# Kernel tuning notes

Hardware: AMD Instinct MI355X
Metric: run time of the kernel (lower is better)

The kernel has to match this reference:

```python
import jax, jax.numpy as jnp
import numpy as np

MAX_OBJECTS = 65536
K = 8            # slots_per_object
D = 256          # d_memory
M = 65536        # number of objects stored this frame (unique indices)


def setup_inputs() -> dict:
    key = jax.random.key(0)
    k1, k2, k3, k4, k5 = jax.random.split(key, 5)
    return {
        "memory": jax.random.normal(k1, (MAX_OBJECTS, K, D), dtype=jnp.float32),
        "capture_poses": jax.random.normal(k2, (MAX_OBJECTS, K, 4, 4), dtype=jnp.float32),
        "slot_filled": jnp.zeros((MAX_OBJECTS, K), dtype=bool),
        "slot_count": jax.random.randint(k3, (MAX_OBJECTS,), 0, 9, dtype=jnp.int32),
        "object_indices": jnp.arange(M, dtype=jnp.int32),
        "features": jax.random.normal(k4, (M, D), dtype=jnp.float32),
        "camera_pose": jax.random.normal(k5, (4, 4), dtype=jnp.float32),
    }


def _pose_deltas(camera_pose, stored_poses):
    # camera_pose: (4,4); stored_poses: (M,K,4,4) -> deltas (M,K)
    R_curr = camera_pose[:3, :3]               # (3,3)
    t_curr = camera_pose[:3, 3]                # (3,)
    R_s = stored_poses[:, :, :3, :3]           # (M,K,3,3)
    t_s = stored_poses[:, :, :3, 3]            # (M,K,3)
    # R_curr @ R_s^T per (m,k): [i,l] = sum_j R_curr[i,j] * R_s[m,k,l,j]
    R_diff = jnp.einsum('ij,mklj->mkil', R_curr, R_s)
    eye = jnp.eye(3, dtype=R_diff.dtype)
    rot_delta = jnp.linalg.norm((R_diff - eye).reshape(*R_diff.shape[:2], 9), axis=-1)
    trans_delta = jnp.linalg.norm(t_curr - t_s, axis=-1)
    return rot_delta + trans_delta             # (M,K)


def reference(memory, capture_poses, slot_filled, slot_count, object_indices, features, camera_pose):
    """Vectorized equivalent of store(): per object, fill next slot if not full,
    else evict the slot with the most similar capture pose. Indices are unique,
    so all M updates are independent and match the sequential torch loop."""
    k = memory.shape[1]
    cnt = slot_count[object_indices]                      # (M,)
    stored = capture_poses[object_indices]                # (M,K,4,4)
    deltas = _pose_deltas(camera_pose, stored)            # (M,K)
    evict_slot = jnp.argmin(deltas, axis=-1).astype(cnt.dtype)
    fill_branch = cnt < k                                 # (M,) bool
    slot = jnp.where(fill_branch, cnt, evict_slot)        # (M,)

    mem_new = memory.at[object_indices, slot].set(features)
    poses_new = capture_poses.at[object_indices, slot].set(camera_pose)
    filled_new = slot_filled.at[object_indices, slot].set(True)
    count_new = slot_count.at[object_indices].add(fill_branch.astype(slot_count.dtype))
    return mem_new, poses_new, filled_new, count_new
```

## Files before the change

### kernel.cpp

```cpp
#include <hip/hip_runtime.h>

#define MAXOBJ 65536
#define KSLOTS 8
#define DFEAT 256

typedef float f32x4 __attribute__((ext_vector_type(4)));


__global__ void init_slots_kernel(int* __restrict__ slots, int n) {
    int i = blockIdx.x * blockDim.x + threadIdx.x;
    if (i < n) slots[i] = -1;
}

__global__ void slot_compute_kernel(const float* __restrict__ capture_poses,
                                    const int* __restrict__ slot_count,
                                    const int* __restrict__ object_indices,
                                    const float* __restrict__ camera_pose,
                                    int* __restrict__ slots,
                                    int* __restrict__ srcs,
                                    int M) {
    int m = blockIdx.x * blockDim.x + threadIdx.x;
    if (m >= M) return;
    int obj = object_indices[m];

    float Rc[3][3], tc[3];
#pragma unroll
    for (int i = 0; i < 3; i++) {
        Rc[i][0] = camera_pose[i * 4 + 0];
        Rc[i][1] = camera_pose[i * 4 + 1];
        Rc[i][2] = camera_pose[i * 4 + 2];
        tc[i]    = camera_pose[i * 4 + 3];
    }

    int cnt = slot_count[obj];
    const float* ps = capture_poses + (size_t)obj * (KSLOTS * 16);

    float best = 3.4e38f;
    int bestk = 0;
#pragma unroll
    for (int k = 0; k < KSLOTS; k++) {
        const float* p = ps + k * 16;
        float rot = 0.f;
#pragma unroll
        for (int i = 0; i < 3; i++) {
#pragma unroll
            for (int l = 0; l < 3; l++) {
                float v = Rc[i][0] * p[l * 4 + 0] + Rc[i][1] * p[l * 4 + 1] + Rc[i][2] * p[l * 4 + 2];
                v -= (i == l) ? 1.f : 0.f;
                rot += v * v;
            }
        }
        float tx = tc[0] - p[3];
        float ty = tc[1] - p[7];
        float tz = tc[2] - p[11];
        float delta = sqrtf(rot) + sqrtf(tx * tx + ty * ty + tz * tz);
        if (delta < best) { best = delta; bestk = k; }
    }

    int fill = (cnt < KSLOTS) ? 1 : 0;
    int slot = fill ? cnt : bestk;
    slots[obj] = slot;
    srcs[obj] = m;
}

__global__ void fused_copy_kernel(const f32x4* __restrict__ memory,
                                  const f32x4* __restrict__ features,
                                  const f32x4* __restrict__ capture_poses,
                                  const f32x4* __restrict__ camera_pose,
                                  const unsigned char* __restrict__ slot_filled,
                                  const int* __restrict__ slot_count,
                                  const int* __restrict__ slots,
                                  const int* __restrict__ srcs,
                                  f32x4* __restrict__ mem_out,
                                  f32x4* __restrict__ poses_out,
                                  float* __restrict__ filled_out,
                                  float* __restrict__ count_out) {
    const int obj = blockIdx.x;
    const int t = threadIdx.x;
    const int slot = slots[obj];
    const int src  = srcs[obj];

    const size_t base = (size_t)obj * (KSLOTS * DFEAT / 4);
    const int d4 = t & 63;

    {
        const int k = t >> 6;
        f32x4 v;
        if (k == slot) {
            v = features[(size_t)src * (DFEAT / 4) + d4];
        } else {
            v = __builtin_nontemporal_load(&memory[base + t]);
        }
        __builtin_nontemporal_store(v, &mem_out[base + t]);
    }
    {
        const int k = 4 + (t >> 6);
        f32x4 v;
        if (k == slot) {
            v = features[(size_t)src * (DFEAT / 4) + d4];
        } else {
            v = __builtin_nontemporal_load(&memory[base + 256 + t]);
        }
        __builtin_nontemporal_store(v, &mem_out[base + 256 + t]);
    }

    if (t < 32) {
        const int k  = t >> 2;
        const int r4 = t & 3;
        const size_t pbase = (size_t)obj * (KSLOTS * 16 / 4);
        f32x4 v = (k == slot) ? camera_pose[r4] : capture_poses[pbase + t];
        poses_out[pbase + t] = v;
    }

    if (t >= 64 && t < 64 + KSLOTS) {
        const int k = t - 64;
        int was = slot_filled[obj * KSLOTS + k] != 0;
        filled_out[obj * KSLOTS + k] = (was || k == slot) ? 1.0f : 0.0f;
    }

    if (t == 96) {
        int cnt = slot_count[obj];
        int fill = (slot >= 0 && cnt < KSLOTS) ? 1 : 0;
        count_out[obj] = (float)(cnt + fill);
    }
}

extern "C" void kernel_launch(void* const* d_in, const int* in_sizes, int n_in,
                              void* d_out, int out_size, void* d_ws, size_t ws_size,
                              hipStream_t stream) {
    const float*         memory        = (const float*)d_in[0];
    const float*         capture_poses = (const float*)d_in[1];
    const unsigned char* slot_filled   = (const unsigned char*)d_in[2];
    const int*           slot_count    = (const int*)d_in[3];
    const int*           object_indices= (const int*)d_in[4];
    const float*         features      = (const float*)d_in[5];
    const float*         camera_pose   = (const float*)d_in[6];
    const int M = in_sizes[4];

    float* out = (float*)d_out;
    float* mem_out    = out;
    float* poses_out  = out + (size_t)MAXOBJ * KSLOTS * DFEAT;
    float* filled_out = poses_out + (size_t)MAXOBJ * KSLOTS * 16;
    float* count_out  = filled_out + (size_t)MAXOBJ * KSLOTS;

    int* slots = (int*)d_ws;
    int* srcs  = slots + MAXOBJ;

    const int B = 256;

    init_slots_kernel<<<(MAXOBJ + B - 1) / B, B, 0, stream>>>(slots, MAXOBJ);

    slot_compute_kernel<<<(M + B - 1) / B, B, 0, stream>>>(
        capture_poses, slot_count, object_indices, camera_pose, slots, srcs, M);

    fused_copy_kernel<<<MAXOBJ, B, 0, stream>>>(
        (const f32x4*)memory, (const f32x4*)features,
        (const f32x4*)capture_poses, (const f32x4*)camera_pose,
        slot_filled, slot_count, slots, srcs,
        (f32x4*)mem_out, (f32x4*)poses_out, filled_out, count_out);
}
```

Measured before the change: 209.9 us.

## Fuse slot selection into copy kernel with warp-shuffle argmin

```diff
diff --git a/kernel.cpp b/kernel.cpp
--- a/kernel.cpp
+++ b/kernel.cpp
@@ -7,121 +7,114 @@
 typedef float f32x4 __attribute__((ext_vector_type(4)));
 
 
-__global__ void init_slots_kernel(int* __restrict__ slots, int n) {
+__global__ void init_srcs_kernel(int* __restrict__ srcs, int n) {
     int i = blockIdx.x * blockDim.x + threadIdx.x;
-    if (i < n) slots[i] = -1;
+    if (i < n) srcs[i] = -1;
 }
 
-__global__ void slot_compute_kernel(const float* __restrict__ capture_poses,
-                                    const int* __restrict__ slot_count,
-                                    const int* __restrict__ object_indices,
-                                    const float* __restrict__ camera_pose,
-                                    int* __restrict__ slots,
-                                    int* __restrict__ srcs,
-                                    int M) {
+__global__ void scatter_srcs_kernel(const int* __restrict__ object_indices,
+                                    int* __restrict__ srcs, int M) {
     int m = blockIdx.x * blockDim.x + threadIdx.x;
-    if (m >= M) return;
-    int obj = object_indices[m];
+    if (m < M) srcs[object_indices[m]] = m;
+}
 
-    float Rc[3][3], tc[3];
+__global__ void fused_kernel(const f32x4* __restrict__ memory,
+                             const f32x4* __restrict__ features,
+                             const f32x4* __restrict__ capture_poses,
+                             const float* __restrict__ camera_pose,
+                             const unsigned char* __restrict__ slot_filled,
+                             const int* __restrict__ slot_count,
+                             const int* __restrict__ srcs,
+                             f32x4* __restrict__ mem_out,
+                             f32x4* __restrict__ poses_out,
+                             float* __restrict__ filled_out,
+                             float* __restrict__ count_out) {
+    const int obj = blockIdx.x;
+    const int t = threadIdx.x;
+    const int src = srcs[obj];
+    const int d4 = t & 63;
+
+    f32x4 feat = {0.f, 0.f, 0.f, 0.f};
+    if (src >= 0) feat = features[(size_t)src * (DFEAT / 4) + d4];
+
+    __shared__ int s_slot;
+
+    if (t < 32) {
+        const int k  = t >> 2;
+        const int r4 = t & 3;
+        const size_t pbase = (size_t)obj * (KSLOTS * 16 / 4);
+        f32x4 pv = capture_poses[pbase + t];
+
+        float Rc00 = camera_pose[0],  Rc01 = camera_pose[1],  Rc02 = camera_pose[2];
+        float Rc10 = camera_pose[4],  Rc11 = camera_pose[5],  Rc12 = camera_pose[6];
+        float Rc20 = camera_pose[8],  Rc21 = camera_pose[9],  Rc22 = camera_pose[10];
+        float tc0 = camera_pose[3], tc1 = camera_pose[7], tc2 = camera_pose[11];
+
+        float rot_part = 0.f, tr_part = 0.f;
+        if (r4 < 3) {
+            float v0 = Rc00 * pv.x + Rc01 * pv.y + Rc02 * pv.z - (r4 == 0 ? 1.f : 0.f);
+            float v1 = Rc10 * pv.x + Rc11 * pv.y + Rc12 * pv.z - (r4 == 1 ? 1.f : 0.f);
+            float v2 = Rc20 * pv.x + Rc21 * pv.y + Rc22 * pv.z - (r4 == 2 ? 1.f : 0.f);
+            rot_part = v0 * v0 + v1 * v1 + v2 * v2;
+            float tcur = (r4 == 0) ? tc0 : (r4 == 1) ? tc1 : tc2;
+            float dt = tcur - pv.w;
+            tr_part = dt * dt;
+        }
+        rot_part += __shfl_xor(rot_part, 1);
+        tr_part  += __shfl_xor(tr_part, 1);
+        rot_part += __shfl_xor(rot_part, 2);
+        tr_part  += __shfl_xor(tr_part, 2);
+        float delta = sqrtf(rot_part) + sqrtf(tr_part);
+
+        int bestk = k;
+        float bestd = delta;
 #pragma unroll
-    for (int i = 0; i < 3; i++) {
-        Rc[i][0] = camera_pose[i * 4 + 0];
-        Rc[i][1] = camera_pose[i * 4 + 1];
-        Rc[i][2] = camera_pose[i * 4 + 2];
-        tc[i]    = camera_pose[i * 4 + 3];
+        for (int mask = 4; mask <= 16; mask <<= 1) {
+            float od = __shfl_xor(bestd, mask);
+            int   ok = __shfl_xor(bestk, mask);
+            if (od < bestd || (od == bestd && ok < bestk)) { bestd = od; bestk = ok; }
+        }
+
+        const int cnt = slot_count[obj];
+        const int fill = (cnt < KSLOTS) ? 1 : 0;
+        const int slot = (src < 0) ? -1 : (fill ? cnt : bestk);
+
+        if (t == 0) {
+            s_slot = slot;
+            count_out[obj] = (float)(cnt + ((src >= 0) ? fill : 0));
+        }
+        if (t < KSLOTS) {
+            int was = slot_filled[obj * KSLOTS + t] != 0;
+            filled_out[obj * KSLOTS + t] = (was || t == slot) ? 1.0f : 0.0f;
+        }
+        f32x4 pov;
+        if (k == slot) {
+            const f32x4* cp4 = (const f32x4*)camera_pose;
+            pov = cp4[r4];
+        } else {
+            pov = pv;
+        }
+        __builtin_nontemporal_store(pov, &poses_out[pbase + t]);
     }
 
-    int cnt = slot_count[obj];
-    const float* ps = capture_poses + (size_t)obj * (KSLOTS * 16);
-
-    float best = 3.4e38f;
-    int bestk = 0;
-#pragma unroll
-    for (int k = 0; k < KSLOTS; k++) {
-        const float* p = ps + k * 16;
-        float rot = 0.f;
-#pragma unroll
-        for (int i = 0; i < 3; i++) {
-#pragma unroll
-            for (int l = 0; l < 3; l++) {
-                float v = Rc[i][0] * p[l * 4 + 0] + Rc[i][1] * p[l * 4 + 1] + Rc[i][2] * p[l * 4 + 2];
-                v -= (i == l) ? 1.f : 0.f;
-                rot += v * v;
-            }
-        }
-        float tx = tc[0] - p[3];
-        float ty = tc[1] - p[7];
-        float tz = tc[2] - p[11];
-        float delta = sqrtf(rot) + sqrtf(tx * tx + ty * ty + tz * tz);
-        if (delta < best) { best = delta; bestk = k; }
-    }
-
-    int fill = (cnt < KSLOTS) ? 1 : 0;
-    int slot = fill ? cnt : bestk;
-    slots[obj] = slot;
-    srcs[obj] = m;
-}
-
-__global__ void fused_copy_kernel(const f32x4* __restrict__ memory,
-                                  const f32x4* __restrict__ features,
-                                  const f32x4* __restrict__ capture_poses,
-                                  const f32x4* __restrict__ camera_pose,
-                                  const unsigned char* __restrict__ slot_filled,
-                                  const int* __restrict__ slot_count,
-                                  const int* __restrict__ slots,
-                                  const int* __restrict__ srcs,
-                                  f32x4* __restrict__ mem_out,
-                                  f32x4* __restrict__ poses_out,
-                                  float* __restrict__ filled_out,
-                                  float* __restrict__ count_out) {
-    const int obj = blockIdx.x;
-    const int t = threadIdx.x;
-    const int slot = slots[obj];
-    const int src  = srcs[obj];
+    __syncthreads();
+    const int slot = s_slot;
 
     const size_t base = (size_t)obj * (KSLOTS * DFEAT / 4);
-    const int d4 = t & 63;
 
     {
         const int k = t >> 6;
         f32x4 v;
-        if (k == slot) {
-            v = features[(size_t)src * (DFEAT / 4) + d4];
-        } else {
-            v = __builtin_nontemporal_load(&memory[base + t]);
-        }
+        if (k == slot) v = feat;
+        else           v = __builtin_nontemporal_load(&memory[base + t]);
         __builtin_nontemporal_store(v, &mem_out[base + t]);
     }
     {
         const int k = 4 + (t >> 6);
         f32x4 v;
-        if (k == slot) {
-            v = features[(size_t)src * (DFEAT / 4) + d4];
-        } else {
-            v = __builtin_nontemporal_load(&memory[base + 256 + t]);
-        }
+        if (k == slot) v = feat;
+        else           v = __builtin_nontemporal_load(&memory[base + 256 + t]);
         __builtin_nontemporal_store(v, &mem_out[base + 256 + t]);
-    }
-
-    if (t < 32) {
-        const int k  = t >> 2;
-        const int r4 = t & 3;
-        const size_t pbase = (size_t)obj * (KSLOTS * 16 / 4);
-        f32x4 v = (k == slot) ? camera_pose[r4] : capture_poses[pbase + t];
-        poses_out[pbase + t] = v;
-    }
-
-    if (t >= 64 && t < 64 + KSLOTS) {
-        const int k = t - 64;
-        int was = slot_filled[obj * KSLOTS + k] != 0;
-        filled_out[obj * KSLOTS + k] = (was || k == slot) ? 1.0f : 0.0f;
-    }
-
-    if (t == 96) {
-        int cnt = slot_count[obj];
-        int fill = (slot >= 0 && cnt < KSLOTS) ? 1 : 0;
-        count_out[obj] = (float)(cnt + fill);
     }
 }
 
@@ -143,19 +136,18 @@
     float* filled_out = poses_out + (size_t)MAXOBJ * KSLOTS * 16;
     float* count_out  = filled_out + (size_t)MAXOBJ * KSLOTS;
 
-    int* slots = (int*)d_ws;
-    int* srcs  = slots + MAXOBJ;
+    int* srcs = (int*)d_ws;
 
     const int B = 256;
 
-    init_slots_kernel<<<(MAXOBJ + B - 1) / B, B, 0, stream>>>(slots, MAXOBJ);
+    if (M < MAXOBJ) {
+        init_srcs_kernel<<<(MAXOBJ + B - 1) / B, B, 0, stream>>>(srcs, MAXOBJ);
+    }
+    scatter_srcs_kernel<<<(M + B - 1) / B, B, 0, stream>>>(object_indices, srcs, M);
 
-    slot_compute_kernel<<<(M + B - 1) / B, B, 0, stream>>>(
-        capture_poses, slot_count, object_indices, camera_pose, slots, srcs, M);
-
-    fused_copy_kernel<<<MAXOBJ, B, 0, stream>>>(
+    fused_kernel<<<MAXOBJ, B, 0, stream>>>(
         (const f32x4*)memory, (const f32x4*)features,
-        (const f32x4*)capture_poses, (const f32x4*)camera_pose,
-        slot_filled, slot_count, slots, srcs,
+        (const f32x4*)capture_poses, camera_pose,
+        slot_filled, slot_count, srcs,
         (f32x4*)mem_out, (f32x4*)poses_out, filled_out, count_out);
 }
```

After: 190.7 us. -9.2%, faster.
